# Optimization experiments

Hardware: AMD Instinct MI355X
Metric: run time of the kernel (lower is better)

The kernel has to match this reference:

```python
import jax, jax.numpy as jnp
import numpy as np

H = 1024
NH = 16
HD = H // NH  # 64

def setup_inputs() -> dict:
    key = jax.random.key(0)
    ks = jax.random.split(key, 6)
    scale = 0.02
    return {
        "hidden_states": jax.random.normal(ks[0], (2, 2048, H), dtype=jnp.float32),
        "Wq": jax.random.normal(ks[1], (H, H), dtype=jnp.float32) * scale,
        "bq": jnp.zeros((H,), dtype=jnp.float32),
        "Wk": jax.random.normal(ks[2], (H, H), dtype=jnp.float32) * scale,
        "bk": jnp.zeros((H,), dtype=jnp.float32),
        "Wv": jax.random.normal(ks[3], (H, H), dtype=jnp.float32) * scale,
        "bv": jnp.zeros((H,), dtype=jnp.float32),
        "Wo": jax.random.normal(ks[4], (H, H), dtype=jnp.float32) * scale,
        "bo": jnp.zeros((H,), dtype=jnp.float32),
    }

def _split_heads(x):
    # [B,S,H] -> [B,NH,S,HD]
    B, S, _ = x.shape
    return x.reshape(B, S, NH, HD).transpose(0, 2, 1, 3)

def reference(hidden_states, Wq, bq, Wk, bk, Wv, bv, Wo, bo):
    # Linear layers: y = x @ W^T + b (torch nn.Linear convention)
    q = _split_heads(hidden_states @ Wq.T + bq)
    k = _split_heads(hidden_states @ Wk.T + bk)
    v = _split_heads(hidden_states @ Wv.T + bv)
    scores = jnp.einsum("bhqd,bhkd->bhqk", q, k) / jnp.sqrt(jnp.float32(HD))
    probs = jax.nn.softmax(scores, axis=-1)  # dropout is identity in eval mode
    ctx = jnp.einsum("bhqk,bhkd->bhqd", probs, v)
    B, _, S, _ = ctx.shape
    ctx = ctx.transpose(0, 2, 1, 3).reshape(B, S, H)
    return ctx @ Wo.T + bo
```

## Files before the change

### kernel.cpp

```cpp
#include <hip/hip_runtime.h>
#include <hip/hip_bf16.h>

#define H_DIM 1024
#define NHEAD 16
#define HDIM  64
#define BATCH 2
#define SEQ   2048
#define MTOT  (BATCH*SEQ)
#define LOG2E 1.4426950408889634f

typedef _Float16 f16x8 __attribute__((ext_vector_type(8)));
typedef float  f32x4  __attribute__((ext_vector_type(4)));
typedef float  f32x16 __attribute__((ext_vector_type(16)));
typedef short  short8 __attribute__((ext_vector_type(8)));
typedef unsigned uint2v __attribute__((ext_vector_type(2)));
typedef unsigned short u16;

static __device__ __forceinline__ u16 f2h(float f) {
  _Float16 h = (_Float16)f;
  return __builtin_bit_cast(u16, h);
}

static __device__ __forceinline__ void load_lds16(const void* g, void* l) {
  __builtin_amdgcn_global_load_lds(
      (const __attribute__((address_space(1))) unsigned int*)g,
      (__attribute__((address_space(3))) unsigned int*)l, 16, 0, 0);
}

#define N8X (MTOT * H_DIM / 8)
#define N8W (H_DIM * H_DIM / 8)

__global__ __launch_bounds__(256) void conv_all(
    const float* __restrict__ x,  const float* __restrict__ Wq,
    const float* __restrict__ Wk, const float* __restrict__ Wv,
    const float* __restrict__ Wo,
    u16* __restrict__ xb, u16* __restrict__ W3, u16* __restrict__ Wo16) {
  int gi = blockIdx.x * 256 + threadIdx.x;
  const float* src;
  u16* dst;
  int ci;
  if (gi < N8X) {
    src = x; dst = xb; ci = gi;
  } else {
    int j = gi - N8X;
    int which = j >> 17;
    ci = j & (N8W - 1);
    src = which == 0 ? Wq : (which == 1 ? Wk : (which == 2 ? Wv : Wo));
    dst = which < 3 ? W3 + (size_t)which * (N8W * 8) : Wo16;
  }
  float4 a = ((const float4*)src)[ci * 2];
  float4 b = ((const float4*)src)[ci * 2 + 1];
  union { u16 u[8]; short8 s; } r;
  r.u[0] = f2h(a.x); r.u[1] = f2h(a.y); r.u[2] = f2h(a.z); r.u[3] = f2h(a.w);
  r.u[4] = f2h(b.x); r.u[5] = f2h(b.y); r.u[6] = f2h(b.z); r.u[7] = f2h(b.w);
  *(short8*)&dst[ci * 8] = r.s;
}

#define BK 32

__global__ __launch_bounds__(256) void gemm_qkv(
    const u16* __restrict__ Xb, const u16* __restrict__ W3,
    const float* __restrict__ bq, const float* __restrict__ bk2,
    const float* __restrict__ bv,
    u16* __restrict__ qp, u16* __restrict__ kp, u16* __restrict__ vp) {
  __shared__ __align__(16) u16 Al[128 * BK];
  __shared__ __align__(16) u16 Bl[128 * BK];
  const int tid = threadIdx.x;
  const int w = tid >> 6, l = tid & 63, lg = l >> 4, lc = l & 15;
  const int wr = w >> 1, wc = w & 1;
  const int m0 = blockIdx.y * 128, n0 = blockIdx.x * 128;
  const int sr = w * 16 + (l >> 2);
  const int sc = (l & 3) * 8;

  f32x4 acc[4][4];
#pragma unroll
  for (int i = 0; i < 4; i++)
#pragma unroll
    for (int j = 0; j < 4; j++) acc[i][j] = (f32x4){0.f, 0.f, 0.f, 0.f};

  for (int k0 = 0; k0 < H_DIM; k0 += BK) {
    __syncthreads();
    load_lds16(&Xb[(size_t)(m0 + sr) * H_DIM + k0 + sc],      &Al[w * 512]);
    load_lds16(&Xb[(size_t)(m0 + 64 + sr) * H_DIM + k0 + sc], &Al[2048 + w * 512]);
    load_lds16(&W3[(size_t)(n0 + sr) * H_DIM + k0 + sc],      &Bl[w * 512]);
    load_lds16(&W3[(size_t)(n0 + 64 + sr) * H_DIM + k0 + sc], &Bl[2048 + w * 512]);
    __syncthreads();

    f16x8 af[4], bfr[4];
#pragma unroll
    for (int mi = 0; mi < 4; mi++)
      af[mi] = *(const f16x8*)&Al[(wr * 64 + mi * 16 + lc) * BK + lg * 8];
#pragma unroll
    for (int nj = 0; nj < 4; nj++)
      bfr[nj] = *(const f16x8*)&Bl[(wc * 64 + nj * 16 + lc) * BK + lg * 8];
#pragma unroll
    for (int mi = 0; mi < 4; mi++)
#pragma unroll
      for (int nj = 0; nj < 4; nj++)
        acc[mi][nj] = __builtin_amdgcn_mfma_f32_16x16x32_f16(af[mi], bfr[nj],
                                                             acc[mi][nj], 0, 0, 0);
  }

  const int np = n0 >> 10;
  u16* outp = np == 0 ? qp : (np == 1 ? kp : vp);
  const float* bias = np == 0 ? bq : (np == 1 ? bk2 : bv);
  const float scale = np == 0 ? (0.125f * LOG2E) : 1.0f;
  const int nc0 = (n0 & 1023) + wc * 64;
  float bvals[4];
#pragma unroll
  for (int nj = 0; nj < 4; nj++) bvals[nj] = bias[nc0 + nj * 16 + lc];
#pragma unroll
  for (int mi = 0; mi < 4; mi++)
#pragma unroll
    for (int nj = 0; nj < 4; nj++)
#pragma unroll
      for (int r = 0; r < 4; r++) {
        int row = m0 + wr * 64 + mi * 16 + lg * 4 + r;
        outp[(size_t)row * 1024 + nc0 + nj * 16 + lc] =
            f2h((acc[mi][nj][r] + bvals[nj]) * scale);
      }
}

__global__ __launch_bounds__(256) void gemm_oproj(
    const u16* __restrict__ A16, const u16* __restrict__ B16,
    const float* __restrict__ bias, float* __restrict__ out) {
  __shared__ __align__(16) u16 Al[128 * BK];
  __shared__ __align__(16) u16 Bl[128 * BK];
  const int tid = threadIdx.x;
  const int w = tid >> 6, l = tid & 63, lg = l >> 4, lc = l & 15;
  const int wr = w >> 1, wc = w & 1;
  const int m0 = blockIdx.y * 128, n0 = blockIdx.x * 128;
  const int sr = w * 16 + (l >> 2);
  const int sc = (l & 3) * 8;

  f32x4 acc[4][4];
#pragma unroll
  for (int i = 0; i < 4; i++)
#pragma unroll
    for (int j = 0; j < 4; j++) acc[i][j] = (f32x4){0.f, 0.f, 0.f, 0.f};

  for (int k0 = 0; k0 < H_DIM; k0 += BK) {
    __syncthreads();
    load_lds16(&A16[(size_t)(m0 + sr) * H_DIM + k0 + sc],      &Al[w * 512]);
    load_lds16(&A16[(size_t)(m0 + 64 + sr) * H_DIM + k0 + sc], &Al[2048 + w * 512]);
    load_lds16(&B16[(size_t)(n0 + sr) * H_DIM + k0 + sc],      &Bl[w * 512]);
    load_lds16(&B16[(size_t)(n0 + 64 + sr) * H_DIM + k0 + sc], &Bl[2048 + w * 512]);
    __syncthreads();

    f16x8 af[4], bfr[4];
#pragma unroll
    for (int mi = 0; mi < 4; mi++)
      af[mi] = *(const f16x8*)&Al[(wr * 64 + mi * 16 + lc) * BK + lg * 8];
#pragma unroll
    for (int nj = 0; nj < 4; nj++)
      bfr[nj] = *(const f16x8*)&Bl[(wc * 64 + nj * 16 + lc) * BK + lg * 8];
#pragma unroll
    for (int mi = 0; mi < 4; mi++)
#pragma unroll
      for (int nj = 0; nj < 4; nj++)
        acc[mi][nj] = __builtin_amdgcn_mfma_f32_16x16x32_f16(af[mi], bfr[nj],
                                                             acc[mi][nj], 0, 0, 0);
  }

  const int nc0 = n0 + wc * 64;
  float bvals[4];
#pragma unroll
  for (int nj = 0; nj < 4; nj++) bvals[nj] = bias[nc0 + nj * 16 + lc];
#pragma unroll
  for (int mi = 0; mi < 4; mi++)
#pragma unroll
    for (int nj = 0; nj < 4; nj++)
#pragma unroll
      for (int r = 0; r < 4; r++) {
        int row = m0 + wr * 64 + mi * 16 + lg * 4 + r;
        out[(size_t)row * 1024 + nc0 + nj * 16 + lc] = acc[mi][nj][r] + bvals[nj];
      }
}

#define KTILES 16

__global__ __launch_bounds__(256, 4) void attn_mfma7(
    const u16* __restrict__ q, const u16* __restrict__ k,
    const u16* __restrict__ v, u16* __restrict__ Opart,
    float* __restrict__ lpart) {
  __shared__ __align__(16) u16 Ks[64 * 64];
  __shared__ __align__(16) u16 Vt[64 * 64];

  const int tid = threadIdx.x;
  const int w = tid >> 6, l = tid & 63;
  const int l31 = l & 31, l5 = l >> 5;
  const int wg = (blockIdx.x & 7) * 128 + (blockIdx.x >> 3);
  const int qt   = wg & 15;
  const int half = (wg >> 4) & 1;
  const int h    = (wg >> 5) & 15;
  const int b    = wg >> 9;
  const size_t row0 = (size_t)b * SEQ;
  const int grow = qt * 128 + w * 32 + l31;

  f16x8 qf[4];
  {
    const u16* qp = q + (row0 + grow) * H_DIM + h * HDIM + 8 * l5;
#pragma unroll
    for (int dc = 0; dc < 4; dc++)
      qf[dc] = *(const f16x8*)(qp + dc * 16);
  }

  const int c1 = tid + 256;
  const u16* ksrc0 = k + (row0 + half * 1024 + (tid >> 3)) * H_DIM + h * HDIM
                       + ((tid & 7) ^ ((tid >> 3) & 7)) * 8;
  const u16* ksrc1 = k + (row0 + half * 1024 + (c1 >> 3)) * H_DIM + h * HDIM
                       + ((c1 & 7) ^ ((c1 >> 3) & 7)) * 8;

  const int vd = tid & 63, ko = tid >> 6;
  const u16* vsrc = v + (row0 + half * 1024 + ko * 8) * H_DIM + h * HDIM + vd;
  const int vwo0 = vd * 64 + ((ko)     ^ (vd & 7)) * 8;
  const int vwo1 = vd * 64 + ((ko + 4) ^ (vd & 7)) * 8;

  uint4 rV0, rV1;
  {
    unsigned a0 = vsrc[0 * H_DIM], a1 = vsrc[1 * H_DIM];
    unsigned a2 = vsrc[2 * H_DIM], a3 = vsrc[3 * H_DIM];
    unsigned a4 = vsrc[4 * H_DIM], a5 = vsrc[5 * H_DIM];
    unsigned a6 = vsrc[6 * H_DIM], a7 = vsrc[7 * H_DIM];
    rV0.x = a0 | (a1 << 16); rV0.y = a2 | (a3 << 16);
    rV0.z = a4 | (a5 << 16); rV0.w = a6 | (a7 << 16);
    const u16* v2 = vsrc + 32 * H_DIM;
    unsigned b0 = v2[0 * H_DIM], b1 = v2[1 * H_DIM];
    unsigned b2 = v2[2 * H_DIM], b3 = v2[3 * H_DIM];
    unsigned b4 = v2[4 * H_DIM], b5 = v2[5 * H_DIM];
    unsigned b6 = v2[6 * H_DIM], b7 = v2[7 * H_DIM];
    rV1.x = b0 | (b1 << 16); rV1.y = b2 | (b3 << 16);
    rV1.z = b4 | (b5 << 16); rV1.w = b6 | (b7 << 16);
  }

  f32x16 Oacc[2];
#pragma unroll
  for (int i = 0; i < 2; i++)
#pragma unroll
    for (int r = 0; r < 16; r++) Oacc[i][r] = 0.f;
  float lS = 0.f;

  for (int t = 0; t < KTILES; ++t) {
    __syncthreads();
    load_lds16(ksrc0, &Ks[w * 512]);
    load_lds16(ksrc1, &Ks[2048 + w * 512]);
    *(uint4*)&Vt[vwo0] = rV0;
    *(uint4*)&Vt[vwo1] = rV1;
    __syncthreads();
    ksrc0 += 64 * H_DIM;
    ksrc1 += 64 * H_DIM;

    if (t + 1 < KTILES) {
      vsrc += 64 * H_DIM;
      unsigned a0 = vsrc[0 * H_DIM], a1 = vsrc[1 * H_DIM];
      unsigned a2 = vsrc[2 * H_DIM], a3 = vsrc[3 * H_DIM];
      unsigned a4 = vsrc[4 * H_DIM], a5 = vsrc[5 * H_DIM];
      unsigned a6 = vsrc[6 * H_DIM], a7 = vsrc[7 * H_DIM];
      rV0.x = a0 | (a1 << 16); rV0.y = a2 | (a3 << 16);
      rV0.z = a4 | (a5 << 16); rV0.w = a6 | (a7 << 16);
      const u16* v2 = vsrc + 32 * H_DIM;
      unsigned b0 = v2[0 * H_DIM], b1 = v2[1 * H_DIM];
      unsigned b2 = v2[2 * H_DIM], b3 = v2[3 * H_DIM];
      unsigned b4 = v2[4 * H_DIM], b5 = v2[5 * H_DIM];
      unsigned b6 = v2[6 * H_DIM], b7 = v2[7 * H_DIM];
      rV1.x = b0 | (b1 << 16); rV1.y = b2 | (b3 << 16);
      rV1.z = b4 | (b5 << 16); rV1.w = b6 | (b7 << 16);
    }

    unsigned pw[2][4][2];
    float ps = 0.f;
#pragma unroll
    for (int kc = 0; kc < 2; kc++) {
      f32x16 s;
#pragma unroll
      for (int r = 0; r < 16; r++) s[r] = 0.f;
      const int key = kc * 32 + l31;
      const int rowb = key * 64, keyx = key & 7;
#pragma unroll
      for (int dc = 0; dc < 4; dc++) {
        f16x8 af = *(const f16x8*)&Ks[rowb + (((dc << 1) + l5) ^ keyx) * 8];
        s = __builtin_amdgcn_mfma_f32_32x32x16_f16(af, qf[dc], s, 0, 0, 0);
      }
#pragma unroll
      for (int rh = 0; rh < 4; rh++)
#pragma unroll
        for (int k1 = 0; k1 < 2; k1++) {
          float e0 = exp2f(s[4 * rh + 2 * k1]);
          float e1 = exp2f(s[4 * rh + 2 * k1 + 1]);
          ps += e0 + e1;
          pw[kc][rh][k1] = __builtin_bit_cast(
              unsigned, __builtin_amdgcn_cvt_pkrtz(e0, e1));
        }
    }
    lS += ps;

#pragma unroll
    for (int kcc = 0; kcc < 4; kcc++) {
      union { unsigned u[4]; f16x8 v8; } bf;
      const int kcs = kcc >> 1, rhA = (kcc & 1) << 1;
#pragma unroll
      for (int k1 = 0; k1 < 2; k1++) {
        uint2v xy = __builtin_amdgcn_permlane32_swap(
            pw[kcs][rhA][k1], pw[kcs][rhA + 1][k1], false, false);
        bf.u[k1] = xy.x;
        bf.u[2 + k1] = xy.y;
      }
#pragma unroll
      for (int dc2 = 0; dc2 < 2; dc2++) {
        const int d = dc2 * 32 + l31;
        f16x8 vf = *(const f16x8*)&Vt[d * 64 + (((kcc << 1) + l5) ^ (d & 7)) * 8];
        Oacc[dc2] = __builtin_amdgcn_mfma_f32_32x32x16_f16(vf, bf.v8,
                                                           Oacc[dc2], 0, 0, 0);
      }
    }
  }

  lS += __shfl_xor(lS, 32);
  u16* ob = Opart + ((size_t)half * MTOT + row0 + grow) * H_DIM + h * HDIM;
#pragma unroll
  for (int dc2 = 0; dc2 < 2; dc2++)
#pragma unroll
    for (int rh = 0; rh < 4; rh++) {
      int d0 = dc2 * 32 + 8 * rh + 4 * l5;
      uint2 pd;
      pd.x = __builtin_bit_cast(unsigned, __builtin_amdgcn_cvt_pkrtz(
          Oacc[dc2][4 * rh + 0], Oacc[dc2][4 * rh + 1]));
      pd.y = __builtin_bit_cast(unsigned, __builtin_amdgcn_cvt_pkrtz(
          Oacc[dc2][4 * rh + 2], Oacc[dc2][4 * rh + 3]));
      *(uint2*)&ob[d0] = pd;
    }
  if (l < 32)
    lpart[((size_t)half * NHEAD + h) * MTOT + row0 + grow] = lS;
}

__global__ __launch_bounds__(256) void combine_kernel(
    const u16* __restrict__ Opart, const float* __restrict__ lpart,
    u16* __restrict__ ctx) {
  int gi = blockIdx.x * 256 + threadIdx.x;
  int r  = gi >> 7;
  int d0 = (gi & 127) * 8;
  int hh = d0 >> 6;
  float lt = lpart[(size_t)hh * MTOT + r] + lpart[(size_t)(NHEAD + hh) * MTOT + r];
  float inv = 1.f / lt;
  short8 a = *(const short8*)&Opart[(size_t)r * H_DIM + d0];
  short8 c = *(const short8*)&Opart[(size_t)MTOT * H_DIM + (size_t)r * H_DIM + d0];
  union { u16 u[8]; short8 s; } rr;
#pragma unroll
  for (int j = 0; j < 8; j++) {
    float fa = (float)__builtin_bit_cast(_Float16, (u16)a[j]);
    float fc = (float)__builtin_bit_cast(_Float16, (u16)c[j]);
    rr.u[j] = f2h((fa + fc) * inv);
  }
  *(short8*)&ctx[(size_t)gi * 8] = rr.s;
}

extern "C" void kernel_launch(void* const* d_in, const int* in_sizes, int n_in,
                              void* d_out, int out_size, void* d_ws, size_t ws_size,
                              hipStream_t stream) {
  const float* x  = (const float*)d_in[0];
  const float* Wq = (const float*)d_in[1];
  const float* bq = (const float*)d_in[2];
  const float* Wk = (const float*)d_in[3];
  const float* bk = (const float*)d_in[4];
  const float* Wv = (const float*)d_in[5];
  const float* bv = (const float*)d_in[6];
  const float* Wo = (const float*)d_in[7];
  const float* bo = (const float*)d_in[8];
  float* out = (float*)d_out;

  const size_t PL = (size_t)MTOT * H_DIM;
  const size_t WN = (size_t)H_DIM * H_DIM;
  u16* xb    = (u16*)d_ws;
  u16* W3    = xb + PL;
  u16* qp    = W3 + 3 * WN;
  u16* kp    = qp + PL;
  u16* vp    = kp + PL;
  u16* ctxp  = vp + PL;
  u16* Wo16  = ctxp + PL;
  u16* Opart = Wo16 + WN;
  float* lpart = (float*)(Opart + 2 * PL);

  conv_all<<<(N8X + 4 * N8W) / 256, 256, 0, stream>>>(
      x, Wq, Wk, Wv, Wo, xb, W3, Wo16);

  gemm_qkv<<<dim3(3072 / 128, MTOT / 128), 256, 0, stream>>>(
      xb, W3, bq, bk, bv, qp, kp, vp);

  attn_mfma7<<<dim3(1024), 256, 0, stream>>>(qp, kp, vp, Opart, lpart);

  combine_kernel<<<dim3((MTOT * H_DIM / 8) / 256), 256, 0, stream>>>(
      Opart, lpart, ctxp);

  gemm_oproj<<<dim3(1024 / 128, MTOT / 128), 256, 0, stream>>>(
      ctxp, Wo16, bo, out);
}
```

Baseline: 137.4 us.

## Split attention keys into four partitions and add a new LDS swizzle

The attention kernel now splits the key range into four 512-key chunks instead of two 1024-key halves. That doubles the grid to 2048 blocks, halves per-block loop length, and raises the launch-bounds occupancy hint. The K/V LDS swizzle is also changed to mix higher key/row bits, aiming to reduce bank conflicts. The combine kernel sums four partial outputs and denominators, which doubles Opart workspace traffic in exchange for more parallelism and occupancy.

```diff
diff --git a/kernel.cpp b/kernel.cpp
--- a/kernel.cpp
+++ b/kernel.cpp
@@ -177,9 +177,9 @@
       }
 }
 
-#define KTILES 16
-
-__global__ __launch_bounds__(256, 4) void attn_mfma7(
+#define KTILES 8
+
+__global__ __launch_bounds__(256, 8) void attn_mfma8(
     const u16* __restrict__ q, const u16* __restrict__ k,
     const u16* __restrict__ v, u16* __restrict__ Opart,
     float* __restrict__ lpart) {
@@ -189,13 +189,14 @@
   const int tid = threadIdx.x;
   const int w = tid >> 6, l = tid & 63;
   const int l31 = l & 31, l5 = l >> 5;
-  const int wg = (blockIdx.x & 7) * 128 + (blockIdx.x >> 3);
-  const int qt   = wg & 15;
-  const int half = (wg >> 4) & 1;
-  const int h    = (wg >> 5) & 15;
-  const int b    = wg >> 9;
+  const int wg = (blockIdx.x & 7) * 256 + (blockIdx.x >> 3);
+  const int qt      = wg & 15;
+  const int quarter = (wg >> 4) & 3;
+  const int h       = (wg >> 6) & 15;
+  const int b       = wg >> 10;
   const size_t row0 = (size_t)b * SEQ;
   const int grow = qt * 128 + w * 32 + l31;
+  const int Ck = (l31 & 7) ^ (((l31 >> 3) & 3) << 1);
 
   f16x8 qf[4];
   {
@@ -205,16 +206,19 @@
       qf[dc] = *(const f16x8*)(qp + dc * 16);
   }
 
+  const int kkey0 = tid >> 3;
   const int c1 = tid + 256;
-  const u16* ksrc0 = k + (row0 + half * 1024 + (tid >> 3)) * H_DIM + h * HDIM
-                       + ((tid & 7) ^ ((tid >> 3) & 7)) * 8;
-  const u16* ksrc1 = k + (row0 + half * 1024 + (c1 >> 3)) * H_DIM + h * HDIM
-                       + ((c1 & 7) ^ ((c1 >> 3) & 7)) * 8;
+  const int kkey1 = c1 >> 3;
+  const u16* ksrc0 = k + (row0 + quarter * 512 + kkey0) * H_DIM + h * HDIM
+      + (((tid & 7) ^ (kkey0 & 7) ^ (((kkey0 >> 3) & 3) << 1)) * 8);
+  const u16* ksrc1 = k + (row0 + quarter * 512 + kkey1) * H_DIM + h * HDIM
+      + (((c1 & 7) ^ (kkey1 & 7) ^ (((kkey1 >> 3) & 3) << 1)) * 8);
 
   const int vd = tid & 63, ko = tid >> 6;
-  const u16* vsrc = v + (row0 + half * 1024 + ko * 8) * H_DIM + h * HDIM + vd;
-  const int vwo0 = vd * 64 + ((ko)     ^ (vd & 7)) * 8;
-  const int vwo1 = vd * 64 + ((ko + 4) ^ (vd & 7)) * 8;
+  const int Cv = (vd & 7) ^ (((vd >> 3) & 3) << 1);
+  const u16* vsrc = v + (row0 + quarter * 512 + ko * 8) * H_DIM + h * HDIM + vd;
+  const int vwo0 = vd * 64 + ((ko)     ^ Cv) * 8;
+  const int vwo1 = vd * 64 + ((ko + 4) ^ Cv) * 8;
 
   uint4 rV0, rV1;
   {
@@ -274,11 +278,10 @@
       f32x16 s;
 #pragma unroll
       for (int r = 0; r < 16; r++) s[r] = 0.f;
-      const int key = kc * 32 + l31;
-      const int rowb = key * 64, keyx = key & 7;
+      const int rowb = (kc * 32 + l31) * 64;
 #pragma unroll
       for (int dc = 0; dc < 4; dc++) {
-        f16x8 af = *(const f16x8*)&Ks[rowb + (((dc << 1) + l5) ^ keyx) * 8];
+        f16x8 af = *(const f16x8*)&Ks[rowb + (((dc << 1) + l5) ^ Ck) * 8];
         s = __builtin_amdgcn_mfma_f32_32x32x16_f16(af, qf[dc], s, 0, 0, 0);
       }
 #pragma unroll
@@ -307,8 +310,8 @@
       }
 #pragma unroll
       for (int dc2 = 0; dc2 < 2; dc2++) {
-        const int d = dc2 * 32 + l31;
-        f16x8 vf = *(const f16x8*)&Vt[d * 64 + (((kcc << 1) + l5) ^ (d & 7)) * 8];
+        const int rowb = (dc2 * 32 + l31) * 64;
+        f16x8 vf = *(const f16x8*)&Vt[rowb + (((kcc << 1) + l5) ^ Ck) * 8];
         Oacc[dc2] = __builtin_amdgcn_mfma_f32_32x32x16_f16(vf, bf.v8,
                                                            Oacc[dc2], 0, 0, 0);
       }
@@ -316,7 +319,7 @@
   }
 
   lS += __shfl_xor(lS, 32);
-  u16* ob = Opart + ((size_t)half * MTOT + row0 + grow) * H_DIM + h * HDIM;
+  u16* ob = Opart + ((size_t)quarter * MTOT + row0 + grow) * H_DIM + h * HDIM;
 #pragma unroll
   for (int dc2 = 0; dc2 < 2; dc2++)
 #pragma unroll
@@ -330,7 +333,7 @@
       *(uint2*)&ob[d0] = pd;
     }
   if (l < 32)
-    lpart[((size_t)half * NHEAD + h) * MTOT + row0 + grow] = lS;
+    lpart[((size_t)quarter * NHEAD + h) * MTOT + row0 + grow] = lS;
 }
 
 __global__ __launch_bounds__(256) void combine_kernel(
@@ -340,17 +343,22 @@
   int r  = gi >> 7;
   int d0 = (gi & 127) * 8;
   int hh = d0 >> 6;
-  float lt = lpart[(size_t)hh * MTOT + r] + lpart[(size_t)(NHEAD + hh) * MTOT + r];
+  float lt = 0.f;
+#pragma unroll
+  for (int p = 0; p < 4; p++)
+    lt += lpart[((size_t)p * NHEAD + hh) * MTOT + r];
   float inv = 1.f / lt;
-  short8 a = *(const short8*)&Opart[(size_t)r * H_DIM + d0];
-  short8 c = *(const short8*)&Opart[(size_t)MTOT * H_DIM + (size_t)r * H_DIM + d0];
+  float acc[8] = {};
+#pragma unroll
+  for (int p = 0; p < 4; p++) {
+    short8 a = *(const short8*)&Opart[((size_t)p * MTOT + r) * H_DIM + d0];
+#pragma unroll
+    for (int j = 0; j < 8; j++)
+      acc[j] += (float)__builtin_bit_cast(_Float16, (u16)a[j]);
+  }
   union { u16 u[8]; short8 s; } rr;
 #pragma unroll
-  for (int j = 0; j < 8; j++) {
-    float fa = (float)__builtin_bit_cast(_Float16, (u16)a[j]);
-    float fc = (float)__builtin_bit_cast(_Float16, (u16)c[j]);
-    rr.u[j] = f2h((fa + fc) * inv);
-  }
+  for (int j = 0; j < 8; j++) rr.u[j] = f2h(acc[j] * inv);
   *(short8*)&ctx[(size_t)gi * 8] = rr.s;
 }
 
@@ -378,7 +386,7 @@
   u16* ctxp  = vp + PL;
   u16* Wo16  = ctxp + PL;
   u16* Opart = Wo16 + WN;
-  float* lpart = (float*)(Opart + 2 * PL);
+  float* lpart = (float*)(Opart + 4 * PL);
 
   conv_all<<<(N8X + 4 * N8W) / 256, 256, 0, stream>>>(
       x, Wq, Wk, Wv, Wo, xb, W3, Wo16);
@@ -386,7 +394,7 @@
   gemm_qkv<<<dim3(3072 / 128, MTOT / 128), 256, 0, stream>>>(
       xb, W3, bq, bk, bv, qp, kp, vp);
 
-  attn_mfma7<<<dim3(1024), 256, 0, stream>>>(qp, kp, vp, Opart, lpart);
+  attn_mfma8<<<dim3(2048), 256, 0, stream>>>(qp, kp, vp, Opart, lpart);
 
   combine_kernel<<<dim3((MTOT * H_DIM / 8) / 256), 256, 0, stream>>>(
       Opart, lpart, ctxp);
```

After: 491.3 us. 3.57x slower.

## Load K fragments directly to registers and double-buffer V tile in LDS

Applied to the files above, without the earlier changes.

The attention kernel drops the shared K tile. Each wave now loads its K MFMA operands straight from global memory into registers and prefetches the next tile after the QK product. V moves to a double-buffered LDS tile with a new XOR swizzle, so each iteration needs one barrier instead of two and the loads of tile t+1/t+2 can overlap compute. The cost is more registers and redundant global K reads across the four waves, which may reduce occupancy or raise L2 traffic.

```diff
diff --git a/kernel.cpp b/kernel.cpp
--- a/kernel.cpp
+++ b/kernel.cpp
@@ -179,12 +179,11 @@
 
 #define KTILES 16
 
-__global__ __launch_bounds__(256, 4) void attn_mfma7(
+__global__ __launch_bounds__(256, 4) void attn_mfma9(
     const u16* __restrict__ q, const u16* __restrict__ k,
     const u16* __restrict__ v, u16* __restrict__ Opart,
     float* __restrict__ lpart) {
-  __shared__ __align__(16) u16 Ks[64 * 64];
-  __shared__ __align__(16) u16 Vt[64 * 64];
+  __shared__ __align__(16) u16 Vt[2][64 * 64];
 
   const int tid = threadIdx.x;
   const int w = tid >> 6, l = tid & 63;
@@ -196,6 +195,7 @@
   const int b    = wg >> 9;
   const size_t row0 = (size_t)b * SEQ;
   const int grow = qt * 128 + w * 32 + l31;
+  const int Ck = (l31 & 7) ^ (((l31 >> 3) & 3) << 1);
 
   f16x8 qf[4];
   {
@@ -205,18 +205,22 @@
       qf[dc] = *(const f16x8*)(qp + dc * 16);
   }
 
-  const int c1 = tid + 256;
-  const u16* ksrc0 = k + (row0 + half * 1024 + (tid >> 3)) * H_DIM + h * HDIM
-                       + ((tid & 7) ^ ((tid >> 3) & 7)) * 8;
-  const u16* ksrc1 = k + (row0 + half * 1024 + (c1 >> 3)) * H_DIM + h * HDIM
-                       + ((c1 & 7) ^ ((c1 >> 3) & 7)) * 8;
+  const u16* kptr = k + (row0 + half * 1024 + l31) * H_DIM + h * HDIM + 8 * l5;
 
   const int vd = tid & 63, ko = tid >> 6;
+  const int Cv = (vd & 7) ^ (((vd >> 3) & 3) << 1);
   const u16* vsrc = v + (row0 + half * 1024 + ko * 8) * H_DIM + h * HDIM + vd;
-  const int vwo0 = vd * 64 + ((ko)     ^ (vd & 7)) * 8;
-  const int vwo1 = vd * 64 + ((ko + 4) ^ (vd & 7)) * 8;
-
+  const int vwo0 = vd * 64 + ((ko)     ^ Cv) * 8;
+  const int vwo1 = vd * 64 + ((ko + 4) ^ Cv) * 8;
+
+  f16x8 kf[2][4];
   uint4 rV0, rV1;
+
+#pragma unroll
+  for (int kc = 0; kc < 2; kc++)
+#pragma unroll
+    for (int dc = 0; dc < 4; dc++)
+      kf[kc][dc] = *(const f16x8*)(kptr + kc * 32 * H_DIM + dc * 16);
   {
     unsigned a0 = vsrc[0 * H_DIM], a1 = vsrc[1 * H_DIM];
     unsigned a2 = vsrc[2 * H_DIM], a3 = vsrc[3 * H_DIM];
@@ -232,6 +236,25 @@
     rV1.x = b0 | (b1 << 16); rV1.y = b2 | (b3 << 16);
     rV1.z = b4 | (b5 << 16); rV1.w = b6 | (b7 << 16);
   }
+  *(uint4*)&Vt[0][vwo0] = rV0;
+  *(uint4*)&Vt[0][vwo1] = rV1;
+  {
+    const u16* vs = vsrc + 64 * H_DIM;
+    unsigned a0 = vs[0 * H_DIM], a1 = vs[1 * H_DIM];
+    unsigned a2 = vs[2 * H_DIM], a3 = vs[3 * H_DIM];
+    unsigned a4 = vs[4 * H_DIM], a5 = vs[5 * H_DIM];
+    unsigned a6 = vs[6 * H_DIM], a7 = vs[7 * H_DIM];
+    rV0.x = a0 | (a1 << 16); rV0.y = a2 | (a3 << 16);
+    rV0.z = a4 | (a5 << 16); rV0.w = a6 | (a7 << 16);
+    const u16* v2 = vs + 32 * H_DIM;
+    unsigned b0 = v2[0 * H_DIM], b1 = v2[1 * H_DIM];
+    unsigned b2 = v2[2 * H_DIM], b3 = v2[3 * H_DIM];
+    unsigned b4 = v2[4 * H_DIM], b5 = v2[5 * H_DIM];
+    unsigned b6 = v2[6 * H_DIM], b7 = v2[7 * H_DIM];
+    rV1.x = b0 | (b1 << 16); rV1.y = b2 | (b3 << 16);
+    rV1.z = b4 | (b5 << 16); rV1.w = b6 | (b7 << 16);
+  }
+  __syncthreads();
 
   f32x16 Oacc[2];
 #pragma unroll
@@ -241,31 +264,7 @@
   float lS = 0.f;
 
   for (int t = 0; t < KTILES; ++t) {
-    __syncthreads();
-    load_lds16(ksrc0, &Ks[w * 512]);
-    load_lds16(ksrc1, &Ks[2048 + w * 512]);
-    *(uint4*)&Vt[vwo0] = rV0;
-    *(uint4*)&Vt[vwo1] = rV1;
-    __syncthreads();
-    ksrc0 += 64 * H_DIM;
-    ksrc1 += 64 * H_DIM;
-
-    if (t + 1 < KTILES) {
-      vsrc += 64 * H_DIM;
-      unsigned a0 = vsrc[0 * H_DIM], a1 = vsrc[1 * H_DIM];
-      unsigned a2 = vsrc[2 * H_DIM], a3 = vsrc[3 * H_DIM];
-      unsigned a4 = vsrc[4 * H_DIM], a5 = vsrc[5 * H_DIM];
-      unsigned a6 = vsrc[6 * H_DIM], a7 = vsrc[7 * H_DIM];
-      rV0.x = a0 | (a1 << 16); rV0.y = a2 | (a3 << 16);
-      rV0.z = a4 | (a5 << 16); rV0.w = a6 | (a7 << 16);
-      const u16* v2 = vsrc + 32 * H_DIM;
-      unsigned b0 = v2[0 * H_DIM], b1 = v2[1 * H_DIM];
-      unsigned b2 = v2[2 * H_DIM], b3 = v2[3 * H_DIM];
-      unsigned b4 = v2[4 * H_DIM], b5 = v2[5 * H_DIM];
-      unsigned b6 = v2[6 * H_DIM], b7 = v2[7 * H_DIM];
-      rV1.x = b0 | (b1 << 16); rV1.y = b2 | (b3 << 16);
-      rV1.z = b4 | (b5 << 16); rV1.w = b6 | (b7 << 16);
-    }
+    const int cur = t & 1;
 
     unsigned pw[2][4][2];
     float ps = 0.f;
@@ -274,13 +273,9 @@
       f32x16 s;
 #pragma unroll
       for (int r = 0; r < 16; r++) s[r] = 0.f;
-      const int key = kc * 32 + l31;
-      const int rowb = key * 64, keyx = key & 7;
-#pragma unroll
-      for (int dc = 0; dc < 4; dc++) {
-        f16x8 af = *(const f16x8*)&Ks[rowb + (((dc << 1) + l5) ^ keyx) * 8];
-        s = __builtin_amdgcn_mfma_f32_32x32x16_f16(af, qf[dc], s, 0, 0, 0);
-      }
+#pragma unroll
+      for (int dc = 0; dc < 4; dc++)
+        s = __builtin_amdgcn_mfma_f32_32x32x16_f16(kf[kc][dc], qf[dc], s, 0, 0, 0);
 #pragma unroll
       for (int rh = 0; rh < 4; rh++)
 #pragma unroll
@@ -294,6 +289,35 @@
     }
     lS += ps;
 
+    if (t + 1 < KTILES) {
+      const u16* kp2 = kptr + (size_t)(t + 1) * 64 * H_DIM;
+#pragma unroll
+      for (int kc = 0; kc < 2; kc++)
+#pragma unroll
+        for (int dc = 0; dc < 4; dc++)
+          kf[kc][dc] = *(const f16x8*)(kp2 + kc * 32 * H_DIM + dc * 16);
+    }
+    if (t + 1 < KTILES) {
+      *(uint4*)&Vt[cur ^ 1][vwo0] = rV0;
+      *(uint4*)&Vt[cur ^ 1][vwo1] = rV1;
+    }
+    if (t + 2 < KTILES) {
+      const u16* vs = vsrc + (size_t)(t + 2) * 64 * H_DIM;
+      unsigned a0 = vs[0 * H_DIM], a1 = vs[1 * H_DIM];
+      unsigned a2 = vs[2 * H_DIM], a3 = vs[3 * H_DIM];
+      unsigned a4 = vs[4 * H_DIM], a5 = vs[5 * H_DIM];
+      unsigned a6 = vs[6 * H_DIM], a7 = vs[7 * H_DIM];
+      rV0.x = a0 | (a1 << 16); rV0.y = a2 | (a3 << 16);
+      rV0.z = a4 | (a5 << 16); rV0.w = a6 | (a7 << 16);
+      const u16* v2 = vs + 32 * H_DIM;
+      unsigned b0 = v2[0 * H_DIM], b1 = v2[1 * H_DIM];
+      unsigned b2 = v2[2 * H_DIM], b3 = v2[3 * H_DIM];
+      unsigned b4 = v2[4 * H_DIM], b5 = v2[5 * H_DIM];
+      unsigned b6 = v2[6 * H_DIM], b7 = v2[7 * H_DIM];
+      rV1.x = b0 | (b1 << 16); rV1.y = b2 | (b3 << 16);
+      rV1.z = b4 | (b5 << 16); rV1.w = b6 | (b7 << 16);
+    }
+
 #pragma unroll
     for (int kcc = 0; kcc < 4; kcc++) {
       union { unsigned u[4]; f16x8 v8; } bf;
@@ -307,12 +331,13 @@
       }
 #pragma unroll
       for (int dc2 = 0; dc2 < 2; dc2++) {
-        const int d = dc2 * 32 + l31;
-        f16x8 vf = *(const f16x8*)&Vt[d * 64 + (((kcc << 1) + l5) ^ (d & 7)) * 8];
+        const int rowb = (dc2 * 32 + l31) * 64;
+        f16x8 vf = *(const f16x8*)&Vt[cur][rowb + (((kcc << 1) + l5) ^ Ck) * 8];
         Oacc[dc2] = __builtin_amdgcn_mfma_f32_32x32x16_f16(vf, bf.v8,
                                                            Oacc[dc2], 0, 0, 0);
       }
     }
+    __syncthreads();
   }
 
   lS += __shfl_xor(lS, 32);
@@ -340,7 +365,8 @@
   int r  = gi >> 7;
   int d0 = (gi & 127) * 8;
   int hh = d0 >> 6;
-  float lt = lpart[(size_t)hh * MTOT + r] + lpart[(size_t)(NHEAD + hh) * MTOT + r];
+  float lt = lpart[(size_t)hh * MTOT + r] +
+             lpart[((size_t)NHEAD + hh) * MTOT + r];
   float inv = 1.f / lt;
   short8 a = *(const short8*)&Opart[(size_t)r * H_DIM + d0];
   short8 c = *(const short8*)&Opart[(size_t)MTOT * H_DIM + (size_t)r * H_DIM + d0];
@@ -386,7 +412,7 @@
   gemm_qkv<<<dim3(3072 / 128, MTOT / 128), 256, 0, stream>>>(
       xb, W3, bq, bk, bv, qp, kp, vp);
 
-  attn_mfma7<<<dim3(1024), 256, 0, stream>>>(qp, kp, vp, Opart, lpart);
+  attn_mfma9<<<dim3(1024), 256, 0, stream>>>(qp, kp, vp, Opart, lpart);
 
   combine_kernel<<<dim3((MTOT * H_DIM / 8) / 256), 256, 0, stream>>>(
       Opart, lpart, ctxp);
```

Result: slower. 167.3 us (+21.7%).

## Fuse split-KV combine and normalization into output projection GEMM A-tile load

Applied to the files above, without the earlier changes.

Removes the separate combine kernel. The O-projection GEMM now reads both partial attention outputs, sums them and scales them by the inverse softmax denominator in fp16 while staging the A tile into LDS. To limit fp16 overflow, Wo is pre-scaled by 1/8 during conversion and the inverse is multiplied by 8. This drops one launch and the ctx write/read round trip. In exchange, A-loads become synchronous register loads instead of direct-to-LDS, and the arithmetic moves into fp16, which may cost some precision.

```diff
diff --git a/kernel.cpp b/kernel.cpp
--- a/kernel.cpp
+++ b/kernel.cpp
@@ -39,6 +39,7 @@
   const float* src;
   u16* dst;
   int ci;
+  float scale = 1.0f;
   if (gi < N8X) {
     src = x; dst = xb; ci = gi;
   } else {
@@ -47,12 +48,15 @@
     ci = j & (N8W - 1);
     src = which == 0 ? Wq : (which == 1 ? Wk : (which == 2 ? Wv : Wo));
     dst = which < 3 ? W3 + (size_t)which * (N8W * 8) : Wo16;
+    if (which == 3) scale = 0.125f;
   }
   float4 a = ((const float4*)src)[ci * 2];
   float4 b = ((const float4*)src)[ci * 2 + 1];
   union { u16 u[8]; short8 s; } r;
-  r.u[0] = f2h(a.x); r.u[1] = f2h(a.y); r.u[2] = f2h(a.z); r.u[3] = f2h(a.w);
-  r.u[4] = f2h(b.x); r.u[5] = f2h(b.y); r.u[6] = f2h(b.z); r.u[7] = f2h(b.w);
+  r.u[0] = f2h(a.x * scale); r.u[1] = f2h(a.y * scale);
+  r.u[2] = f2h(a.z * scale); r.u[3] = f2h(a.w * scale);
+  r.u[4] = f2h(b.x * scale); r.u[5] = f2h(b.y * scale);
+  r.u[6] = f2h(b.z * scale); r.u[7] = f2h(b.w * scale);
   *(short8*)&dst[ci * 8] = r.s;
 }
 
@@ -121,8 +125,9 @@
       }
 }
 
-__global__ __launch_bounds__(256) void gemm_oproj(
-    const u16* __restrict__ A16, const u16* __restrict__ B16,
+__global__ __launch_bounds__(256) void gemm_oproj_fused(
+    const u16* __restrict__ Op0, const u16* __restrict__ Op1,
+    const float* __restrict__ lpart, const u16* __restrict__ B16,
     const float* __restrict__ bias, float* __restrict__ out) {
   __shared__ __align__(16) u16 Al[128 * BK];
   __shared__ __align__(16) u16 Bl[128 * BK];
@@ -139,27 +144,45 @@
 #pragma unroll
     for (int j = 0; j < 4; j++) acc[i][j] = (f32x4){0.f, 0.f, 0.f, 0.f};
 
-  for (int k0 = 0; k0 < H_DIM; k0 += BK) {
-    __syncthreads();
-    load_lds16(&A16[(size_t)(m0 + sr) * H_DIM + k0 + sc],      &Al[w * 512]);
-    load_lds16(&A16[(size_t)(m0 + 64 + sr) * H_DIM + k0 + sc], &Al[2048 + w * 512]);
-    load_lds16(&B16[(size_t)(n0 + sr) * H_DIM + k0 + sc],      &Bl[w * 512]);
-    load_lds16(&B16[(size_t)(n0 + 64 + sr) * H_DIM + k0 + sc], &Bl[2048 + w * 512]);
-    __syncthreads();
-
-    f16x8 af[4], bfr[4];
-#pragma unroll
-    for (int mi = 0; mi < 4; mi++)
-      af[mi] = *(const f16x8*)&Al[(wr * 64 + mi * 16 + lc) * BK + lg * 8];
-#pragma unroll
-    for (int nj = 0; nj < 4; nj++)
-      bfr[nj] = *(const f16x8*)&Bl[(wc * 64 + nj * 16 + lc) * BK + lg * 8];
-#pragma unroll
-    for (int mi = 0; mi < 4; mi++)
+  for (int head = 0; head < NHEAD; head++) {
+    float lt0 = lpart[(size_t)head * MTOT + m0 + sr] +
+                lpart[((size_t)NHEAD + head) * MTOT + m0 + sr];
+    float lt1 = lpart[(size_t)head * MTOT + m0 + 64 + sr] +
+                lpart[((size_t)NHEAD + head) * MTOT + m0 + 64 + sr];
+    _Float16 iv0 = (_Float16)(8.0f / lt0);
+    _Float16 iv1 = (_Float16)(8.0f / lt1);
+    f16x8 iv0v = {iv0, iv0, iv0, iv0, iv0, iv0, iv0, iv0};
+    f16x8 iv1v = {iv1, iv1, iv1, iv1, iv1, iv1, iv1, iv1};
+#pragma unroll
+    for (int kk = 0; kk < 2; kk++) {
+      const int k0 = head * 64 + kk * 32;
+      __syncthreads();
+      load_lds16(&B16[(size_t)(n0 + sr) * H_DIM + k0 + sc],      &Bl[w * 512]);
+      load_lds16(&B16[(size_t)(n0 + 64 + sr) * H_DIM + k0 + sc], &Bl[2048 + w * 512]);
+      f16x8 a0 = *(const f16x8*)&Op0[(size_t)(m0 + sr) * H_DIM + k0 + sc];
+      f16x8 a1 = *(const f16x8*)&Op1[(size_t)(m0 + sr) * H_DIM + k0 + sc];
+      f16x8 c0 = (a0 + a1) * iv0v;
+      f16x8 b0 = *(const f16x8*)&Op0[(size_t)(m0 + 64 + sr) * H_DIM + k0 + sc];
+      f16x8 b1 = *(const f16x8*)&Op1[(size_t)(m0 + 64 + sr) * H_DIM + k0 + sc];
+      f16x8 c1 = (b0 + b1) * iv1v;
+      *(f16x8*)&Al[tid * 8] = c0;
+      *(f16x8*)&Al[2048 + tid * 8] = c1;
+      __syncthreads();
+
+      f16x8 af[4], bfr[4];
+#pragma unroll
+      for (int mi = 0; mi < 4; mi++)
+        af[mi] = *(const f16x8*)&Al[(wr * 64 + mi * 16 + lc) * BK + lg * 8];
 #pragma unroll
       for (int nj = 0; nj < 4; nj++)
-        acc[mi][nj] = __builtin_amdgcn_mfma_f32_16x16x32_f16(af[mi], bfr[nj],
-                                                             acc[mi][nj], 0, 0, 0);
+        bfr[nj] = *(const f16x8*)&Bl[(wc * 64 + nj * 16 + lc) * BK + lg * 8];
+#pragma unroll
+      for (int mi = 0; mi < 4; mi++)
+#pragma unroll
+        for (int nj = 0; nj < 4; nj++)
+          acc[mi][nj] = __builtin_amdgcn_mfma_f32_16x16x32_f16(af[mi], bfr[nj],
+                                                               acc[mi][nj], 0, 0, 0);
+    }
   }
 
   const int nc0 = n0 + wc * 64;
@@ -333,27 +356,6 @@
     lpart[((size_t)half * NHEAD + h) * MTOT + row0 + grow] = lS;
 }
 
-__global__ __launch_bounds__(256) void combine_kernel(
-    const u16* __restrict__ Opart, const float* __restrict__ lpart,
-    u16* __restrict__ ctx) {
-  int gi = blockIdx.x * 256 + threadIdx.x;
-  int r  = gi >> 7;
-  int d0 = (gi & 127) * 8;
-  int hh = d0 >> 6;
-  float lt = lpart[(size_t)hh * MTOT + r] + lpart[(size_t)(NHEAD + hh) * MTOT + r];
-  float inv = 1.f / lt;
-  short8 a = *(const short8*)&Opart[(size_t)r * H_DIM + d0];
-  short8 c = *(const short8*)&Opart[(size_t)MTOT * H_DIM + (size_t)r * H_DIM + d0];
-  union { u16 u[8]; short8 s; } rr;
-#pragma unroll
-  for (int j = 0; j < 8; j++) {
-    float fa = (float)__builtin_bit_cast(_Float16, (u16)a[j]);
-    float fc = (float)__builtin_bit_cast(_Float16, (u16)c[j]);
-    rr.u[j] = f2h((fa + fc) * inv);
-  }
-  *(short8*)&ctx[(size_t)gi * 8] = rr.s;
-}
-
 extern "C" void kernel_launch(void* const* d_in, const int* in_sizes, int n_in,
                               void* d_out, int out_size, void* d_ws, size_t ws_size,
                               hipStream_t stream) {
@@ -375,8 +377,7 @@
   u16* qp    = W3 + 3 * WN;
   u16* kp    = qp + PL;
   u16* vp    = kp + PL;
-  u16* ctxp  = vp + PL;
-  u16* Wo16  = ctxp + PL;
+  u16* Wo16  = vp + PL;
   u16* Opart = Wo16 + WN;
   float* lpart = (float*)(Opart + 2 * PL);
 
@@ -388,9 +389,6 @@
 
   attn_mfma7<<<dim3(1024), 256, 0, stream>>>(qp, kp, vp, Opart, lpart);
 
-  combine_kernel<<<dim3((MTOT * H_DIM / 8) / 256), 256, 0, stream>>>(
-      Opart, lpart, ctxp);
-
-  gemm_oproj<<<dim3(1024 / 128, MTOT / 128), 256, 0, stream>>>(
-      ctxp, Wo16, bo, out);
-}
+  gemm_oproj_fused<<<dim3(1024 / 128, MTOT / 128), 256, 0, stream>>>(
+      Opart, Opart + PL, lpart, Wo16, bo, out);
+}
```

New measurement: 143.3 us. 4.2% more time.
